# Kernel optimization log

Hardware: AMD Instinct MI355X
Metric: run time of the kernel (lower is better)

## Reference

```python
import jax, jax.numpy as jnp
import numpy as np

COMMITMENT_COST = 0.25
EPS = 1e-12  # matches torch F.normalize default eps


def _l2norm(v, axis=-1):
    n = jnp.linalg.norm(v, axis=axis, keepdims=True)
    return v / jnp.maximum(n, EPS)


def setup_inputs() -> dict:
    key = jax.random.key(0)
    k1, k2 = jax.random.split(key)
    x = jax.random.normal(k1, (65536, 256), dtype=jnp.float32)
    codebook = jax.random.normal(k2, (4096, 256), dtype=jnp.float32)
    return {"x": x, "codebook": codebook}


def reference(x, codebook):
    # x: [N, D] latents; codebook: [K, D] embedding table
    xn = _l2norm(x)                 # [N, D]
    cbn = _l2norm(codebook)         # [K, D]

    # Squared L2 distances: ||xn||^2 + ||cbn||^2 - 2 xn.cbn^T  -> [N, K]
    dists = (
        jnp.sum(xn * xn, axis=-1, keepdims=True)
        + jnp.sum(cbn * cbn, axis=1)
        - 2.0 * jnp.einsum("nd,kd->nk", xn, cbn)
    )
    idx = jnp.argmin(dists, axis=1)  # [N]

    # quantize: gather then L2-normalize (matches F.normalize(embeddings(idx)))
    quantized = _l2norm(cbn[idx])    # [N, D]

    q_latent_loss = jnp.mean((quantized - jax.lax.stop_gradient(xn)) ** 2)
    e_latent_loss = jnp.mean((xn - jax.lax.stop_gradient(quantized)) ** 2)
    loss = q_latent_loss + COMMITMENT_COST * e_latent_loss

    # straight-through estimator
    quantized_st = xn + jax.lax.stop_gradient(quantized - xn)
    return quantized_st, loss, idx
```

## Files before the change

kernel.cpp:

```cpp
#include <hip/hip_runtime.h>
#include <math.h>

#define N_ROWS 65536
#define DIM    256
#define NCODE  4096
#define MARGIN 2e-4f
#define TILE_C 32
#define NTILE  (NCODE / TILE_C)
#define FB     4
#define FIXG   512

typedef __attribute__((ext_vector_type(8)))  short short8v;
typedef __attribute__((ext_vector_type(4)))  float float4v;
typedef __attribute__((ext_vector_type(16))) float f32x16;

__device__ inline unsigned short f2bf(float f) {
    unsigned u = __float_as_uint(f);
    unsigned r = (u + 0x7fffu + ((u >> 16) & 1u)) >> 16;
    return (unsigned short)r;
}
__device__ inline float bf2f(unsigned short h) {
    return __uint_as_float(((unsigned)h) << 16);
}
__device__ inline void gll16(const void* g, void* l) {
    __builtin_amdgcn_global_load_lds(
        (const __attribute__((address_space(1))) unsigned int*)g,
        (__attribute__((address_space(3))) unsigned int*)l, 16, 0, 0);
}

__global__ void cb_norm_kernel(const float* __restrict__ cb,
                               float* __restrict__ cbn,
                               unsigned short* __restrict__ pk,
                               float* __restrict__ c2,
                               double* __restrict__ c2d,
                               double* __restrict__ ndi) {
    int k = blockIdx.x;
    int t = threadIdx.x;
    float v = cb[k * DIM + t];
    double dv = (double)v;
    double ss = dv * dv;
    __shared__ double red2[4], red3[4], redn[4];
    #pragma unroll
    for (int off = 32; off > 0; off >>= 1) ss += __shfl_down(ss, off);
    if ((t & 63) == 0) redn[t >> 6] = ss;
    __syncthreads();
    double S = redn[0] + redn[1] + redn[2] + redn[3];
    double nrm = fmax(sqrt(S), 1e-12);
    double cq = dv / nrm;
    float cf = (float)cq;
    cbn[k * DIM + t] = cf;
    unsigned short hb = f2bf(cf);
    unsigned short lb = f2bf(cf - bf2f(hb));
    {
        int cb32 = k >> 5, klo = k & 31, ks = t >> 4, hi = (t >> 3) & 1, j = t & 7;
        size_t ch = ((size_t)cb32 * 16 + ks) * 2;
        size_t slot = (size_t)(hi * 32 + klo) * 8 + j;
        pk[(ch + 0) * 512 + slot] = hb;
        pk[(ch + 1) * 512 + slot] = lb;
    }
    double s2 = (double)cf * (double)cf;
    double s3 = cq * cq;
    #pragma unroll
    for (int off = 32; off > 0; off >>= 1) {
        s2 += __shfl_down(s2, off);
        s3 += __shfl_down(s3, off);
    }
    if ((t & 63) == 0) { red2[t >> 6] = s2; red3[t >> 6] = s3; }
    __syncthreads();
    if (t == 0) {
        c2[k]  = (float)(red2[0] + red2[1] + red2[2] + red2[3]);
        c2d[k] = red3[0] + red3[1] + red3[2] + red3[3];
        ndi[k] = 1.0 / nrm;
    }
}

__global__ void x_norm_kernel(const float* __restrict__ x,
                              float* __restrict__ nx,
                              float* __restrict__ scx,
                              int* __restrict__ counter) {
    if (blockIdx.x == 0 && threadIdx.x == 0) counter[0] = 0;
    int w = threadIdx.x >> 6;
    int lane = threadIdx.x & 63;
    int row = blockIdx.x * 4 + w;
    float4 v = ((const float4*)(x + (size_t)row * DIM))[lane];
    double ss = (double)v.x * v.x + (double)v.y * v.y
              + (double)v.z * v.z + (double)v.w * v.w;
    #pragma unroll
    for (int off = 32; off > 0; off >>= 1) ss += __shfl_down(ss, off);
    if (lane == 0) {
        double n = fmax(sqrt(ss), 1e-12);
        nx[row]  = (float)n;
        scx[row] = (float)(2.0 / n);
    }
}

__attribute__((amdgpu_waves_per_eu(2, 2)))
__global__ void __launch_bounds__(256)
argmin_mfma_kernel(const float* __restrict__ x,
                   const unsigned short* __restrict__ pk,
                   const float* __restrict__ c2,
                   const float* __restrict__ scx,
                   int* __restrict__ idx_out,
                   int* __restrict__ counter,
                   int* __restrict__ rowlist) {
    __shared__ unsigned short buf[2][16384];

    int tid  = threadIdx.x;
    int lane = tid & 63;
    int wave = tid >> 6;
    int cl31 = lane & 31;
    int hi   = lane >> 5;
    int xbase = blockIdx.x * 128 + wave * 32;

    short8v bh[16], bl[16];
    const float* xr = x + (size_t)(xbase + cl31) * DIM + hi * 8;
    #pragma unroll
    for (int ks = 0; ks < 16; ks++) {
        float4 f0 = *(const float4*)(xr + ks * 16);
        float4 f1 = *(const float4*)(xr + ks * 16 + 4);
        float e[8] = {f0.x, f0.y, f0.z, f0.w, f1.x, f1.y, f1.z, f1.w};
        short8v h, l;
        #pragma unroll
        for (int j = 0; j < 8; j++) {
            unsigned short hb = f2bf(e[j]);
            h[j] = (short)hb;
            l[j] = (short)f2bf(e[j] - bf2f(hb));
        }
        bh[ks] = h;
        bl[ks] = l;
    }
    float scr = scx[xbase + cl31];

    float s1 = 3.4e38f, s2 = 3.4e38f;
    int   i1 = 0x7fffffff;

    {
        const unsigned short* src = pk + ((size_t)wave * 8) * 512 + lane * 8;
        unsigned short* dst = &buf[0][(wave * 8) * 512];
        #pragma unroll
        for (int i = 0; i < 8; i++) gll16(src + i * 512, dst + i * 512);
    }
    __syncthreads();

    int cur = 0;
    for (int t = 0; t < NTILE; t++) {
        int cbb = t * TILE_C;

        if (t + 1 < NTILE) {
            const unsigned short* src =
                pk + ((size_t)(t + 1) * 32 + wave * 8) * 512 + lane * 8;
            unsigned short* dst = &buf[cur ^ 1][(wave * 8) * 512];
            #pragma unroll
            for (int i = 0; i < 8; i++) gll16(src + i * 512, dst + i * 512);
        }

        const unsigned short* cbuf = &buf[cur][0];
        f32x16 acc = {0.f,0.f,0.f,0.f,0.f,0.f,0.f,0.f,0.f,0.f,0.f,0.f,0.f,0.f,0.f,0.f};
        #pragma unroll
        for (int ks = 0; ks < 16; ks++) {
            short8v ah = *(const short8v*)(cbuf + (size_t)(ks * 2 + 0) * 512 + lane * 8);
            short8v al = *(const short8v*)(cbuf + (size_t)(ks * 2 + 1) * 512 + lane * 8);
            acc = __builtin_amdgcn_mfma_f32_32x32x16_bf16(ah, bh[ks], acc, 0, 0, 0);
            acc = __builtin_amdgcn_mfma_f32_32x32x16_bf16(ah, bl[ks], acc, 0, 0, 0);
            acc = __builtin_amdgcn_mfma_f32_32x32x16_bf16(al, bh[ks], acc, 0, 0, 0);
        }

        const float4v* c2p = (const float4v*)(c2 + cbb + hi * 4);
        float4v gq0 = c2p[0], gq1 = c2p[2], gq2 = c2p[4], gq3 = c2p[6];
        float sv[16];
        float mn = 3.4e38f;
        #pragma unroll
        for (int g = 0; g < 4; g++) {
            float4v gg = (g == 0) ? gq0 : (g == 1) ? gq1 : (g == 2) ? gq2 : gq3;
            #pragma unroll
            for (int q = 0; q < 4; q++) {
                float s = gg[q] - scr * acc[g * 4 + q];
                sv[g * 4 + q] = s;
                mn = fminf(mn, s);
            }
        }
        if (!__all(mn >= s2)) {
            #pragma unroll
            for (int g = 0; g < 4; g++) {
                #pragma unroll
                for (int q = 0; q < 4; q++) {
                    float s = sv[g * 4 + q];
                    int ci = cbb + q + 8 * g + 4 * hi;
                    if (s < s1) { s2 = s1; s1 = s; i1 = ci; }
                    else if (s < s2) s2 = s;
                }
            }
        }

        __syncthreads();
        cur ^= 1;
    }

    {
        float o1 = __shfl_xor(s1, 32);
        int   oi = __shfl_xor(i1, 32);
        float o2 = __shfl_xor(s2, 32);
        if (o1 < s1 || (o1 == s1 && oi < i1)) { s2 = fminf(s1, o2); s1 = o1; i1 = oi; }
        else                                   { s2 = fminf(o1, s2); }
    }
    if (lane < 32) {
        int row = xbase + lane;
        idx_out[row] = i1;
        if (s2 - s1 < MARGIN) { int slot = atomicAdd(counter, 1); rowlist[slot] = row; }
    }
}

__global__ void fixup_kernel(const float* __restrict__ x,
                             const float* __restrict__ cb,
                             const double* __restrict__ c2d,
                             const double* __restrict__ ndi,
                             const int* __restrict__ counter,
                             const int* __restrict__ rowlist,
                             int* __restrict__ idxv) {
    __shared__ double xs[FB][DIM];
    __shared__ double isx_sh[FB];
    __shared__ double red_bs[4][FB];
    __shared__ int    red_bi[4][FB];
    int t = threadIdx.x, lane = t & 63, wave = t >> 6;
    int cnt = counter[0];

    for (int base = blockIdx.x * FB; base < cnt; base += FIXG * FB) {
        int nb = cnt - base; if (nb > FB) nb = FB;

        #pragma unroll
        for (int r = 0; r < FB; r++) {
            if (r < nb) {
                int row = rowlist[base + r];
                xs[r][t] = (double)x[(size_t)row * DIM + t];
            }
        }
        __syncthreads();
        if (wave < nb) {
            double a0 = xs[wave][lane],       a1 = xs[wave][lane + 64];
            double a2 = xs[wave][lane + 128], a3 = xs[wave][lane + 192];
            double ss = a0 * a0 + a1 * a1 + a2 * a2 + a3 * a3;
            #pragma unroll
            for (int off = 32; off > 0; off >>= 1) ss += __shfl_down(ss, off);
            if (lane == 0) isx_sh[wave] = 2.0 / fmax(sqrt(ss), 1e-12);
        }
        __syncthreads();

        double isx0 = isx_sh[0], isx1 = isx_sh[1], isx2 = isx_sh[2], isx3 = isx_sh[3];
        double bs0 = 1e300, bs1 = 1e300, bs2 = 1e300, bs3 = 1e300;
        int    bi0 = 0x7fffffff, bi1 = 0x7fffffff, bi2 = 0x7fffffff, bi3 = 0x7fffffff;

        for (int k0 = 0; k0 < NCODE / 256; k0++) {
            int k = k0 * 256 + t;
            const float4* cr = (const float4*)(cb + (size_t)k * DIM);
            double d0 = 0.0, d1 = 0.0, d2 = 0.0, d3 = 0.0;
            #pragma unroll 8
            for (int d4 = 0; d4 < DIM / 4; d4++) {
                float4 c = cr[d4];
                double cx = c.x, cy = c.y, cz = c.z, cw = c.w;
                int d = d4 * 4;
                d0 = fma(cx, xs[0][d], d0); d0 = fma(cy, xs[0][d+1], d0);
                d0 = fma(cz, xs[0][d+2], d0); d0 = fma(cw, xs[0][d+3], d0);
                d1 = fma(cx, xs[1][d], d1); d1 = fma(cy, xs[1][d+1], d1);
                d1 = fma(cz, xs[1][d+2], d1); d1 = fma(cw, xs[1][d+3], d1);
                d2 = fma(cx, xs[2][d], d2); d2 = fma(cy, xs[2][d+1], d2);
                d2 = fma(cz, xs[2][d+2], d2); d2 = fma(cw, xs[2][d+3], d2);
                d3 = fma(cx, xs[3][d], d3); d3 = fma(cy, xs[3][d+1], d3);
                d3 = fma(cz, xs[3][d+2], d3); d3 = fma(cw, xs[3][d+3], d3);
            }
            double ndik = ndi[k], c2k = c2d[k];
            double s0 = c2k - isx0 * d0 * ndik;
            double s1v = c2k - isx1 * d1 * ndik;
            double s2v = c2k - isx2 * d2 * ndik;
            double s3v = c2k - isx3 * d3 * ndik;
            if (s0 < bs0 || (s0 == bs0 && k < bi0)) { bs0 = s0; bi0 = k; }
            if (s1v < bs1 || (s1v == bs1 && k < bi1)) { bs1 = s1v; bi1 = k; }
            if (s2v < bs2 || (s2v == bs2 && k < bi2)) { bs2 = s2v; bi2 = k; }
            if (s3v < bs3 || (s3v == bs3 && k < bi3)) { bs3 = s3v; bi3 = k; }
        }

        #pragma unroll
        for (int m = 1; m < 64; m <<= 1) {
            double os; int oi;
            os = __shfl_xor(bs0, m); oi = __shfl_xor(bi0, m);
            if (os < bs0 || (os == bs0 && oi < bi0)) { bs0 = os; bi0 = oi; }
            os = __shfl_xor(bs1, m); oi = __shfl_xor(bi1, m);
            if (os < bs1 || (os == bs1 && oi < bi1)) { bs1 = os; bi1 = oi; }
            os = __shfl_xor(bs2, m); oi = __shfl_xor(bi2, m);
            if (os < bs2 || (os == bs2 && oi < bi2)) { bs2 = os; bi2 = oi; }
            os = __shfl_xor(bs3, m); oi = __shfl_xor(bi3, m);
            if (os < bs3 || (os == bs3 && oi < bi3)) { bs3 = os; bi3 = oi; }
        }
        if (lane == 0) {
            red_bs[wave][0] = bs0; red_bi[wave][0] = bi0;
            red_bs[wave][1] = bs1; red_bi[wave][1] = bi1;
            red_bs[wave][2] = bs2; red_bi[wave][2] = bi2;
            red_bs[wave][3] = bs3; red_bi[wave][3] = bi3;
        }
        __syncthreads();
        if (t < nb) {
            double b = red_bs[0][t]; int idx = red_bi[0][t];
            #pragma unroll
            for (int w = 1; w < 4; w++) {
                double ob = red_bs[w][t]; int oi = red_bi[w][t];
                if (ob < b || (ob == b && oi < idx)) { b = ob; idx = oi; }
            }
            idxv[rowlist[base + t]] = idx;
        }
        __syncthreads();
    }
}

__global__ void gather_loss_kernel(const float* __restrict__ x,
                                   const float* __restrict__ cbn,
                                   const float* __restrict__ c2,
                                   const float* __restrict__ nx,
                                   const int* __restrict__ idxv,
                                   float* __restrict__ out_q,
                                   float* __restrict__ out_idxf,
                                   float* __restrict__ partials) {
    int w = threadIdx.x >> 6, lane = threadIdx.x & 63;
    int row = blockIdx.x * 4 + w;
    int iv = idxv[row];
    float inv_qn = 1.0f / fmaxf(sqrtf(c2[iv]), 1e-12f);
    float inx = 1.0f / nx[row];
    float4 q4 = ((const float4*)(cbn + (size_t)iv * DIM))[lane];
    float4 x4 = ((const float4*)(x + (size_t)row * DIM))[lane];
    float4 qq;
    qq.x = q4.x * inv_qn; qq.y = q4.y * inv_qn;
    qq.z = q4.z * inv_qn; qq.w = q4.w * inv_qn;
    ((float4*)(out_q + (size_t)row * DIM))[lane] = qq;
    float dx = qq.x - x4.x * inx;
    float dy = qq.y - x4.y * inx;
    float dz = qq.z - x4.z * inx;
    float dw = qq.w - x4.w * inx;
    float ss = dx * dx + dy * dy + dz * dz + dw * dw;
    #pragma unroll
    for (int off = 32; off > 0; off >>= 1) ss += __shfl_down(ss, off);
    if (lane == 0) {
        partials[row] = ss;
        out_idxf[row] = (float)iv;
    }
}

__global__ void loss_reduce_kernel(const float* __restrict__ partials,
                                   float* __restrict__ out_loss) {
    int t = threadIdx.x;
    float s = 0.0f;
    for (int i = t; i < N_ROWS; i += 256) s += partials[i];
    __shared__ float red[4];
    #pragma unroll
    for (int off = 32; off > 0; off >>= 1) s += __shfl_down(s, off);
    if ((t & 63) == 0) red[t >> 6] = s;
    __syncthreads();
    if (t == 0) out_loss[0] = 1.25f * (red[0] + red[1] + red[2] + red[3]) / (float)(N_ROWS * DIM);
}

extern "C" void kernel_launch(void* const* d_in, const int* in_sizes, int n_in,
                              void* d_out, int out_size, void* d_ws, size_t ws_size,
                              hipStream_t stream) {
    const float* x  = (const float*)d_in[0];
    const float* cb = (const float*)d_in[1];
    float* out = (float*)d_out;

    double* c2d = (double*)d_ws;
    double* ndi = c2d + NCODE;
    float* cbn = (float*)(ndi + NCODE);
    float* c2  = cbn + (size_t)NCODE * DIM;
    float* nx  = c2 + NCODE;
    float* scx = nx + N_ROWS;
    int*   idxv = (int*)(scx + N_ROWS);
    float* partials = (float*)(idxv + N_ROWS);
    int*   counter  = (int*)(partials + N_ROWS);
    int*   rowlist  = counter + 4;
    unsigned short* pk = (unsigned short*)(rowlist + N_ROWS);

    float* out_q    = out;
    float* out_loss = out + (size_t)N_ROWS * DIM;
    float* out_idxf = out_loss + 1;

    hipLaunchKernelGGL(cb_norm_kernel, dim3(NCODE), dim3(256), 0, stream,
                       cb, cbn, pk, c2, c2d, ndi);
    hipLaunchKernelGGL(x_norm_kernel, dim3(N_ROWS / 4), dim3(256), 0, stream, x, nx, scx, counter);
    hipLaunchKernelGGL(argmin_mfma_kernel, dim3(N_ROWS / 128), dim3(256), 0, stream,
                       x, pk, c2, scx, idxv, counter, rowlist);
    hipLaunchKernelGGL(fixup_kernel, dim3(FIXG), dim3(256), 0, stream,
                       x, cb, c2d, ndi, counter, rowlist, idxv);
    hipLaunchKernelGGL(gather_loss_kernel, dim3(N_ROWS / 4), dim3(256), 0, stream,
                       x, cbn, c2, nx, idxv, out_q, out_idxf, partials);
    hipLaunchKernelGGL(loss_reduce_kernel, dim3(1), dim3(256), 0, stream,
                       partials, out_loss);
}
```

Measured before the change: 618.2 us.

## Split fp64 fixup over codebook chunks with merge pass, drop cbn buffer

The fp64 exact re-check of ambiguous rows is split into a 2D work space of row batches (now 8 rows each) times four codebook chunks. Each chunk writes per-row partial minima, and a new merge kernel reduces them into the final index. This exposes more blocks when the ambiguous-row count is small, and each codebook load now feeds more rows. It also stops writing the normalized float codebook and rebuilds quantized vectors in the gather kernel from the raw codebook times the fp64 inverse norm. The costs are an extra launch, partial-result traffic and more registers per thread for the eight accumulators.

```diff
diff --git a/kernel.cpp b/kernel.cpp
--- a/kernel.cpp
+++ b/kernel.cpp
@@ -7,7 +7,9 @@
 #define MARGIN 2e-4f
 #define TILE_C 32
 #define NTILE  (NCODE / TILE_C)
-#define FB     4
+#define FB     8
+#define KCH    1024
+#define NCH    (NCODE / KCH)
 #define FIXG   512
 
 typedef __attribute__((ext_vector_type(8)))  short short8v;
@@ -29,7 +31,6 @@
 }
 
 __global__ void cb_norm_kernel(const float* __restrict__ cb,
-                               float* __restrict__ cbn,
                                unsigned short* __restrict__ pk,
                                float* __restrict__ c2,
                                double* __restrict__ c2d,
@@ -48,7 +49,6 @@
     double nrm = fmax(sqrt(S), 1e-12);
     double cq = dv / nrm;
     float cf = (float)cq;
-    cbn[k * DIM + t] = cf;
     unsigned short hb = f2bf(cf);
     unsigned short lb = f2bf(cf - bf2f(hb));
     {
@@ -210,109 +210,120 @@
     }
 }
 
-__global__ void fixup_kernel(const float* __restrict__ x,
-                             const float* __restrict__ cb,
-                             const double* __restrict__ c2d,
-                             const double* __restrict__ ndi,
-                             const int* __restrict__ counter,
-                             const int* __restrict__ rowlist,
-                             int* __restrict__ idxv) {
+__global__ void fixup2d_kernel(const float* __restrict__ x,
+                               const float* __restrict__ cb,
+                               const double* __restrict__ c2d,
+                               const double* __restrict__ ndi,
+                               const int* __restrict__ counter,
+                               const int* __restrict__ rowlist,
+                               double* __restrict__ pb_s,
+                               int* __restrict__ pb_i) {
     __shared__ double xs[FB][DIM];
     __shared__ double isx_sh[FB];
-    __shared__ double red_bs[4][FB];
-    __shared__ int    red_bi[4][FB];
+    __shared__ double red_s[4][FB];
+    __shared__ int    red_i[4][FB];
     int t = threadIdx.x, lane = t & 63, wave = t >> 6;
     int cnt = counter[0];
-
-    for (int base = blockIdx.x * FB; base < cnt; base += FIXG * FB) {
+    int nbat = (cnt + FB - 1) / FB;
+    int nwork = nbat * NCH;
+
+    for (int w = blockIdx.x; w < nwork; w += FIXG) {
+        int batch = w / NCH, chunk = w - batch * NCH;
+        int base = batch * FB;
         int nb = cnt - base; if (nb > FB) nb = FB;
 
         #pragma unroll
-        for (int r = 0; r < FB; r++) {
-            if (r < nb) {
-                int row = rowlist[base + r];
-                xs[r][t] = (double)x[(size_t)row * DIM + t];
-            }
-        }
+        for (int r = 0; r < FB; r++)
+            if (r < nb) xs[r][t] = (double)x[(size_t)rowlist[base + r] * DIM + t];
         __syncthreads();
-        if (wave < nb) {
-            double a0 = xs[wave][lane],       a1 = xs[wave][lane + 64];
-            double a2 = xs[wave][lane + 128], a3 = xs[wave][lane + 192];
+
+        for (int rr = wave; rr < nb; rr += 4) {
+            double a0 = xs[rr][lane],       a1 = xs[rr][lane + 64];
+            double a2 = xs[rr][lane + 128], a3 = xs[rr][lane + 192];
             double ss = a0 * a0 + a1 * a1 + a2 * a2 + a3 * a3;
             #pragma unroll
-            for (int off = 32; off > 0; off >>= 1) ss += __shfl_down(ss, off);
-            if (lane == 0) isx_sh[wave] = 2.0 / fmax(sqrt(ss), 1e-12);
+            for (int m = 1; m < 64; m <<= 1) ss += __shfl_xor(ss, m);
+            if (lane == 0) isx_sh[rr] = 2.0 / fmax(sqrt(ss), 1e-12);
         }
         __syncthreads();
 
-        double isx0 = isx_sh[0], isx1 = isx_sh[1], isx2 = isx_sh[2], isx3 = isx_sh[3];
-        double bs0 = 1e300, bs1 = 1e300, bs2 = 1e300, bs3 = 1e300;
-        int    bi0 = 0x7fffffff, bi1 = 0x7fffffff, bi2 = 0x7fffffff, bi3 = 0x7fffffff;
-
-        for (int k0 = 0; k0 < NCODE / 256; k0++) {
-            int k = k0 * 256 + t;
+        double bs[FB]; int bi[FB];
+        #pragma unroll
+        for (int r = 0; r < FB; r++) { bs[r] = 1e300; bi[r] = 0x7fffffff; }
+
+        for (int k0 = 0; k0 < KCH / 256; k0++) {
+            int k = chunk * KCH + k0 * 256 + t;
             const float4* cr = (const float4*)(cb + (size_t)k * DIM);
-            double d0 = 0.0, d1 = 0.0, d2 = 0.0, d3 = 0.0;
-            #pragma unroll 8
+            double d[FB];
+            #pragma unroll
+            for (int r = 0; r < FB; r++) d[r] = 0.0;
+            #pragma unroll 4
             for (int d4 = 0; d4 < DIM / 4; d4++) {
                 float4 c = cr[d4];
                 double cx = c.x, cy = c.y, cz = c.z, cw = c.w;
-                int d = d4 * 4;
-                d0 = fma(cx, xs[0][d], d0); d0 = fma(cy, xs[0][d+1], d0);
-                d0 = fma(cz, xs[0][d+2], d0); d0 = fma(cw, xs[0][d+3], d0);
-                d1 = fma(cx, xs[1][d], d1); d1 = fma(cy, xs[1][d+1], d1);
-                d1 = fma(cz, xs[1][d+2], d1); d1 = fma(cw, xs[1][d+3], d1);
-                d2 = fma(cx, xs[2][d], d2); d2 = fma(cy, xs[2][d+1], d2);
-                d2 = fma(cz, xs[2][d+2], d2); d2 = fma(cw, xs[2][d+3], d2);
-                d3 = fma(cx, xs[3][d], d3); d3 = fma(cy, xs[3][d+1], d3);
-                d3 = fma(cz, xs[3][d+2], d3); d3 = fma(cw, xs[3][d+3], d3);
+                int dd = d4 * 4;
+                #pragma unroll
+                for (int r = 0; r < FB; r++) {
+                    d[r] = fma(cx, xs[r][dd],     d[r]);
+                    d[r] = fma(cy, xs[r][dd + 1], d[r]);
+                    d[r] = fma(cz, xs[r][dd + 2], d[r]);
+                    d[r] = fma(cw, xs[r][dd + 3], d[r]);
+                }
             }
             double ndik = ndi[k], c2k = c2d[k];
-            double s0 = c2k - isx0 * d0 * ndik;
-            double s1v = c2k - isx1 * d1 * ndik;
-            double s2v = c2k - isx2 * d2 * ndik;
-            double s3v = c2k - isx3 * d3 * ndik;
-            if (s0 < bs0 || (s0 == bs0 && k < bi0)) { bs0 = s0; bi0 = k; }
-            if (s1v < bs1 || (s1v == bs1 && k < bi1)) { bs1 = s1v; bi1 = k; }
-            if (s2v < bs2 || (s2v == bs2 && k < bi2)) { bs2 = s2v; bi2 = k; }
-            if (s3v < bs3 || (s3v == bs3 && k < bi3)) { bs3 = s3v; bi3 = k; }
-        }
-
-        #pragma unroll
-        for (int m = 1; m < 64; m <<= 1) {
-            double os; int oi;
-            os = __shfl_xor(bs0, m); oi = __shfl_xor(bi0, m);
-            if (os < bs0 || (os == bs0 && oi < bi0)) { bs0 = os; bi0 = oi; }
-            os = __shfl_xor(bs1, m); oi = __shfl_xor(bi1, m);
-            if (os < bs1 || (os == bs1 && oi < bi1)) { bs1 = os; bi1 = oi; }
-            os = __shfl_xor(bs2, m); oi = __shfl_xor(bi2, m);
-            if (os < bs2 || (os == bs2 && oi < bi2)) { bs2 = os; bi2 = oi; }
-            os = __shfl_xor(bs3, m); oi = __shfl_xor(bi3, m);
-            if (os < bs3 || (os == bs3 && oi < bi3)) { bs3 = os; bi3 = oi; }
-        }
-        if (lane == 0) {
-            red_bs[wave][0] = bs0; red_bi[wave][0] = bi0;
-            red_bs[wave][1] = bs1; red_bi[wave][1] = bi1;
-            red_bs[wave][2] = bs2; red_bi[wave][2] = bi2;
-            red_bs[wave][3] = bs3; red_bi[wave][3] = bi3;
+            #pragma unroll
+            for (int r = 0; r < FB; r++) {
+                double sc = c2k - isx_sh[r] * d[r] * ndik;
+                if (sc < bs[r] || (sc == bs[r] && k < bi[r])) { bs[r] = sc; bi[r] = k; }
+            }
+        }
+
+        #pragma unroll
+        for (int r = 0; r < FB; r++) {
+            double b = bs[r]; int idx = bi[r];
+            #pragma unroll
+            for (int m = 1; m < 64; m <<= 1) {
+                double ob = __shfl_xor(b, m);
+                int   oi = __shfl_xor(idx, m);
+                if (ob < b || (ob == b && oi < idx)) { b = ob; idx = oi; }
+            }
+            if (lane == 0) { red_s[wave][r] = b; red_i[wave][r] = idx; }
         }
         __syncthreads();
         if (t < nb) {
-            double b = red_bs[0][t]; int idx = red_bi[0][t];
-            #pragma unroll
-            for (int w = 1; w < 4; w++) {
-                double ob = red_bs[w][t]; int oi = red_bi[w][t];
+            double b = red_s[0][t]; int idx = red_i[0][t];
+            #pragma unroll
+            for (int ww = 1; ww < 4; ww++) {
+                double ob = red_s[ww][t]; int oi = red_i[ww][t];
                 if (ob < b || (ob == b && oi < idx)) { b = ob; idx = oi; }
             }
-            idxv[rowlist[base + t]] = idx;
+            pb_s[(size_t)(base + t) * NCH + chunk] = b;
+            pb_i[(size_t)(base + t) * NCH + chunk] = idx;
         }
         __syncthreads();
     }
 }
 
+__global__ void fixmerge_kernel(const int* __restrict__ counter,
+                                const int* __restrict__ rowlist,
+                                const double* __restrict__ pb_s,
+                                const int* __restrict__ pb_i,
+                                int* __restrict__ idxv) {
+    int cnt = counter[0];
+    for (int s = blockIdx.x * 256 + threadIdx.x; s < cnt; s += gridDim.x * 256) {
+        double b = pb_s[(size_t)s * NCH]; int idx = pb_i[(size_t)s * NCH];
+        #pragma unroll
+        for (int c = 1; c < NCH; c++) {
+            double ob = pb_s[(size_t)s * NCH + c]; int oi = pb_i[(size_t)s * NCH + c];
+            if (ob < b || (ob == b && oi < idx)) { b = ob; idx = oi; }
+        }
+        idxv[rowlist[s]] = idx;
+    }
+}
+
 __global__ void gather_loss_kernel(const float* __restrict__ x,
-                                   const float* __restrict__ cbn,
-                                   const float* __restrict__ c2,
+                                   const float* __restrict__ cb,
+                                   const double* __restrict__ ndi,
                                    const float* __restrict__ nx,
                                    const int* __restrict__ idxv,
                                    float* __restrict__ out_q,
@@ -321,13 +332,13 @@
     int w = threadIdx.x >> 6, lane = threadIdx.x & 63;
     int row = blockIdx.x * 4 + w;
     int iv = idxv[row];
-    float inv_qn = 1.0f / fmaxf(sqrtf(c2[iv]), 1e-12f);
+    float ndif = (float)ndi[iv];
     float inx = 1.0f / nx[row];
-    float4 q4 = ((const float4*)(cbn + (size_t)iv * DIM))[lane];
+    float4 q4 = ((const float4*)(cb + (size_t)iv * DIM))[lane];
     float4 x4 = ((const float4*)(x + (size_t)row * DIM))[lane];
     float4 qq;
-    qq.x = q4.x * inv_qn; qq.y = q4.y * inv_qn;
-    qq.z = q4.z * inv_qn; qq.w = q4.w * inv_qn;
+    qq.x = q4.x * ndif; qq.y = q4.y * ndif;
+    qq.z = q4.z * ndif; qq.w = q4.w * ndif;
     ((float4*)(out_q + (size_t)row * DIM))[lane] = qq;
     float dx = qq.x - x4.x * inx;
     float dy = qq.y - x4.y * inx;
@@ -362,31 +373,34 @@
     const float* cb = (const float*)d_in[1];
     float* out = (float*)d_out;
 
-    double* c2d = (double*)d_ws;
-    double* ndi = c2d + NCODE;
-    float* cbn = (float*)(ndi + NCODE);
-    float* c2  = cbn + (size_t)NCODE * DIM;
-    float* nx  = c2 + NCODE;
-    float* scx = nx + N_ROWS;
-    int*   idxv = (int*)(scx + N_ROWS);
-    float* partials = (float*)(idxv + N_ROWS);
-    int*   counter  = (int*)(partials + N_ROWS);
-    int*   rowlist  = counter + 4;
-    unsigned short* pk = (unsigned short*)(rowlist + N_ROWS);
+    double* c2d  = (double*)d_ws;
+    double* ndi  = c2d + NCODE;
+    double* pb_s = ndi + NCODE;
+    float*  c2   = (float*)(pb_s + (size_t)N_ROWS * NCH);
+    float*  nx   = c2 + NCODE;
+    float*  scx  = nx + N_ROWS;
+    int*    idxv = (int*)(scx + N_ROWS);
+    float*  partials = (float*)(idxv + N_ROWS);
+    int*    counter  = (int*)(partials + N_ROWS);
+    int*    rowlist  = counter + 8;
+    int*    pb_i     = rowlist + N_ROWS;
+    unsigned short* pk = (unsigned short*)(pb_i + (size_t)N_ROWS * NCH);
 
     float* out_q    = out;
     float* out_loss = out + (size_t)N_ROWS * DIM;
     float* out_idxf = out_loss + 1;
 
     hipLaunchKernelGGL(cb_norm_kernel, dim3(NCODE), dim3(256), 0, stream,
-                       cb, cbn, pk, c2, c2d, ndi);
+                       cb, pk, c2, c2d, ndi);
     hipLaunchKernelGGL(x_norm_kernel, dim3(N_ROWS / 4), dim3(256), 0, stream, x, nx, scx, counter);
     hipLaunchKernelGGL(argmin_mfma_kernel, dim3(N_ROWS / 128), dim3(256), 0, stream,
                        x, pk, c2, scx, idxv, counter, rowlist);
-    hipLaunchKernelGGL(fixup_kernel, dim3(FIXG), dim3(256), 0, stream,
-                       x, cb, c2d, ndi, counter, rowlist, idxv);
+    hipLaunchKernelGGL(fixup2d_kernel, dim3(FIXG), dim3(256), 0, stream,
+                       x, cb, c2d, ndi, counter, rowlist, pb_s, pb_i);
+    hipLaunchKernelGGL(fixmerge_kernel, dim3(64), dim3(256), 0, stream,
+                       counter, rowlist, pb_s, pb_i, idxv);
     hipLaunchKernelGGL(gather_loss_kernel, dim3(N_ROWS / 4), dim3(256), 0, stream,
-                       x, cbn, c2, nx, idxv, out_q, out_idxf, partials);
+                       x, cb, ndi, nx, idxv, out_q, out_idxf, partials);
     hipLaunchKernelGGL(loss_reduce_kernel, dim3(1), dim3(256), 0, stream,
                        partials, out_loss);
 }
```

New measurement: 599.3 us. 1.03x faster.
